# Performance work log

Hardware: AMD Instinct MI355X
Metric: run time of the kernel (lower is better)

## Reference

```python
import jax, jax.numpy as jnp
import numpy as np

B, S, D, H = 2, 2048, 1024, 16
HD = D // H  # head_dim = 64
ROPE_BASE = 10000.0


def setup_inputs() -> dict:
    key = jax.random.key(0)
    ks = jax.random.split(key, 5)
    scale = 1.0 / np.sqrt(D)
    return {
        "x": jax.random.normal(ks[0], (B, S, D), dtype=jnp.float32),
        "Wq": jax.random.normal(ks[1], (D, D), dtype=jnp.float32) * scale,
        "Wk": jax.random.normal(ks[2], (D, D), dtype=jnp.float32) * scale,
        "Wv": jax.random.normal(ks[3], (D, D), dtype=jnp.float32) * scale,
        "Wo": jax.random.normal(ks[4], (D, D), dtype=jnp.float32) * scale,
    }


def _rotate_half(x):
    x1, x2 = x[..., : HD // 2], x[..., HD // 2:]
    return jnp.concatenate((-x2, x1), axis=-1)


def _rope_cos_sin(seq_len):
    inv_freq = 1.0 / (ROPE_BASE ** (jnp.arange(0, HD, 2, dtype=jnp.float32) / HD))
    t = jnp.arange(seq_len, dtype=jnp.float32)
    freqs = jnp.outer(t, inv_freq)          # [S, HD/2]
    emb = jnp.concatenate((freqs, freqs), -1)  # [S, HD]
    return jnp.cos(emb), jnp.sin(emb)


def reference(x, Wq, Wk, Wv, Wo):
    # projections (torch Linear: y = x @ W.T), split heads -> [B, H, S, HD]
    def proj(W):
        return (x @ W.T).reshape(B, S, H, HD).transpose(0, 2, 1, 3)

    q, k, v = proj(Wq), proj(Wk), proj(Wv)

    cos, sin = _rope_cos_sin(S)  # [S, HD] each, broadcast over B, H
    q = q * cos + _rotate_half(q) * sin
    k = k * cos + _rotate_half(k) * sin

    scale = 1.0 / np.sqrt(HD)
    scores = jnp.einsum("bhsd,bhtd->bhst", q, k) * scale  # [B,H,S,S]
    attn = jax.nn.softmax(scores, axis=-1)
    out = jnp.einsum("bhst,bhtd->bhsd", attn, v)           # [B,H,S,HD]
    out = out.transpose(0, 2, 1, 3).reshape(B, S, D)
    return out @ Wo.T
```

## Files before the change

### kernel.cpp

```cpp
#include <hip/hip_runtime.h>
#include <hip/hip_bf16.h>
#include <math.h>
#include <stdint.h>

typedef __bf16 bf16;
typedef __bf16 bf16x8 __attribute__((ext_vector_type(8)));
typedef __bf16 bf16x4 __attribute__((ext_vector_type(4)));
typedef float  f32x4  __attribute__((ext_vector_type(4)));
typedef float  f32x16 __attribute__((ext_vector_type(16)));
typedef unsigned int u32x4 __attribute__((ext_vector_type(4)));

#define MFMA16(a,b,c) __builtin_amdgcn_mfma_f32_16x16x32_bf16((a),(b),(c),0,0,0)
#define MFMA32(a,b,c) __builtin_amdgcn_mfma_f32_32x32x16_bf16((a),(b),(c),0,0,0)

static constexpr int kB  = 2;
static constexpr int kS  = 2048;
static constexpr int kD  = 1024;
static constexpr int kH  = 16;
static constexpr int kHD = 64;
static constexpr int kM  = kB * kS;
static constexpr float kExpC = 0.125f * 1.44269504f;

__device__ __forceinline__ void gl_lds16(const bf16* g, bf16* l) {
  __builtin_amdgcn_global_load_lds(
      (const __attribute__((address_space(1))) unsigned int*)g,
      (__attribute__((address_space(3))) unsigned int*)l, 16, 0, 0);
}

__device__ __forceinline__ unsigned cvt_pk_bf16(float lo, float hi) {
  unsigned r;
  asm("v_cvt_pk_bf16_f32 %0, %1, %2" : "=v"(r) : "v"(lo), "v"(hi));
  return r;
}

__global__ void cvt_all(const float* __restrict__ x,
                        const float* __restrict__ wq, const float* __restrict__ wk,
                        const float* __restrict__ wv, const float* __restrict__ wo,
                        bf16* __restrict__ xb,
                        bf16* __restrict__ wqb, bf16* __restrict__ wkb,
                        bf16* __restrict__ wvb, bf16* __restrict__ wob,
                        float2* __restrict__ rtab)
{
  const int i = blockIdx.x * 256 + threadIdx.x;
  const int NX4 = (kM * kD) / 4;
  const int NW4 = (kD * kD) / 4;
  if (i >= NX4 + 4 * NW4) {
    const int idx = i - (NX4 + 4 * NW4);
    const int s = idx >> 5, d = idx & 31;
    const float f = exp2f(-(float)d * 0.4152410118609203f);
    float sn, cs;
    sincosf((float)s * f, &sn, &cs);
    rtab[idx] = make_float2(cs, sn);
    return;
  }
  const float* src; bf16* dst; int off;
  if (i < NX4) { src = x; dst = xb; off = i; }
  else {
    const int j = i - NX4;
    const int seg = j >> 18;
    off = j & (NW4 - 1);
    src = (seg == 0) ? wq : (seg == 1) ? wk : (seg == 2) ? wv : wo;
    dst = (seg == 0) ? wqb : (seg == 1) ? wkb : (seg == 2) ? wvb : wob;
  }
  const float4 v = ((const float4*)src)[off];
  bf16x4 o = { (bf16)v.x, (bf16)v.y, (bf16)v.z, (bf16)v.w };
  ((bf16x4*)dst)[off] = o;
}

__device__ __forceinline__ void gemm_core_128(
    const bf16* __restrict__ A, const bf16* __restrict__ Bw,
    int m0, int n0, int K, bf16* smem, f32x4 acc[4][4])
{
  const int t = threadIdx.x, lane = t & 63, wave = t >> 6;
  const int wm = wave >> 1, wn = wave & 1;
  const int srow = lane >> 2;
  const int scol = (lane & 3) * 8;
  const bf16* ga0 = A  + (size_t)(m0 + wave * 16 + srow) * K + scol;
  const bf16* ga1 = ga0 + (size_t)64 * K;
  const bf16* gb0 = Bw + (size_t)(n0 + wave * 16 + srow) * K + scol;
  const bf16* gb1 = gb0 + (size_t)64 * K;
  const int woff = wave * 512;

  {
    bf16* lb = smem;
    gl_lds16(ga0, lb + woff);
    gl_lds16(ga1, lb + 2048 + woff);
    gl_lds16(gb0, lb + 4096 + woff);
    gl_lds16(gb1, lb + 6144 + woff);
  }
  int cur = 0;
  for (int k0 = 0; k0 < K; k0 += 32) {
    __syncthreads();
    if (k0 + 32 < K) {
      bf16* lb = smem + (cur ^ 1) * 8192;
      gl_lds16(ga0 + k0 + 32, lb + woff);
      gl_lds16(ga1 + k0 + 32, lb + 2048 + woff);
      gl_lds16(gb0 + k0 + 32, lb + 4096 + woff);
      gl_lds16(gb1 + k0 + 32, lb + 6144 + woff);
    }
    const bf16* aT = smem + cur * 8192;
    const bf16* bT = aT + 4096;
    bf16x8 af[4], bfr[4];
#pragma unroll
    for (int i = 0; i < 4; ++i) {
      af[i]  = *(const bf16x8*)(aT + (wm * 64 + i * 16 + (lane & 15)) * 32 + (lane >> 4) * 8);
      bfr[i] = *(const bf16x8*)(bT + (wn * 64 + i * 16 + (lane & 15)) * 32 + (lane >> 4) * 8);
    }
#pragma unroll
    for (int i = 0; i < 4; ++i)
#pragma unroll
      for (int j = 0; j < 4; ++j)
        acc[i][j] = MFMA16(af[i], bfr[j], acc[i][j]);
    cur ^= 1;
  }
}

__global__ __launch_bounds__(256, 4) void proj_qkv(
    const bf16* __restrict__ xb,
    const bf16* __restrict__ wqb, const bf16* __restrict__ wkb, const bf16* __restrict__ wvb,
    bf16* __restrict__ Qb, bf16* __restrict__ Kb, bf16* __restrict__ Vt,
    const float2* __restrict__ rtab)
{
  __shared__ __align__(16) bf16 smem[16384];
  const int z = blockIdx.z;
  const bf16* Ww = (z == 0) ? wqb : (z == 1) ? wkb : wvb;
  const int m0 = blockIdx.x * 128, n0 = blockIdx.y * 128;
  f32x4 acc[4][4] = {};
  gemm_core_128(xb, Ww, m0, n0, kD, smem, acc);

  const int lane = threadIdx.x & 63, wave = threadIdx.x >> 6;
  const int wm = wave >> 1, wn = wave & 1, quad = lane >> 4, lc = lane & 15;
  const int hh = (n0 >> 6) + wn;
  if (z == 2) {
    __syncthreads();
    const int t = threadIdx.x;
    const int row = t >> 1;
    const int coff = (t & 1) * 32;
    const int bidx = m0 >> 11;
    const int hh2 = (n0 >> 6) + (row >> 6);
    const int d = row & 63;
    bf16* vtr = smem;
#pragma unroll
    for (int p = 0; p < 2; ++p) {
      if (p) __syncthreads();
      if (wm == p) {
#pragma unroll
        for (int i = 0; i < 4; ++i)
#pragma unroll
          for (int j = 0; j < 4; ++j) {
            bf16x4 pk;
#pragma unroll
            for (int r = 0; r < 4; ++r) pk[r] = (bf16)acc[i][j][r];
            *(bf16x4*)&vtr[(wn * 64 + j * 16 + lc) * 72 + i * 16 + quad * 4] = pk;
          }
      }
      __syncthreads();
      bf16* dst = Vt + ((size_t)(bidx * kH + hh2) * kHD + d) * kS
                     + (m0 & 2047) + p * 64 + coff;
#pragma unroll
      for (int u = 0; u < 4; ++u)
        *(uint4*)(dst + u * 8) = *(const uint4*)&vtr[row * 72 + coff + u * 8];
    }
  } else {
    bf16* Op = (z == 0) ? Qb : Kb;
    const float f = (z == 0) ? kExpC : 1.0f;
#pragma unroll
    for (int j = 0; j < 2; ++j) {
      const int d = j * 16 + lc;
#pragma unroll
      for (int i = 0; i < 4; ++i)
#pragma unroll
        for (int r = 0; r < 4; ++r) {
          const int m = m0 + wm * 64 + i * 16 + quad * 4 + r;
          const int bidx = m >> 11, s = m & 2047;
          const float2 cs = rtab[s * 32 + d];
          const float v0 = acc[i][j][r], v1 = acc[i][j + 2][r];
          bf16* dst = Op + ((size_t)(bidx * kH + hh) * kS + s) * kHD;
          dst[d]      = (bf16)((v0 * cs.x - v1 * cs.y) * f);
          dst[d + 32] = (bf16)((v1 * cs.x + v0 * cs.y) * f);
        }
    }
  }
}

__global__ __launch_bounds__(256, 2) void attn(
    const bf16* __restrict__ Qb, const bf16* __restrict__ Kb,
    const bf16* __restrict__ Vt, bf16* __restrict__ Ob)
{
  __shared__ __align__(16) bf16 kT2[2][128 * 64];
  __shared__ __align__(16) bf16 vT2[2][64 * 128];
  const int t = threadIdx.x, lane = t & 63, wave = t >> 6;
  const int l31 = lane & 31, hi = lane >> 5;
  const int bid = blockIdx.x;
  const int qt = (bid >> 3) & 15;
  const int bh = (bid & 7) * 4 + (bid >> 7);
  const size_t base = (size_t)bh * kS * kHD;
  const bf16* Qp = Qb + base + (size_t)qt * 128 * kHD;
  const bf16* Kp = Kb + base;
  const bf16* Vp = Vt + base;

  bf16x8 qf[4];
#pragma unroll
  for (int ks = 0; ks < 4; ++ks)
    qf[ks] = *(const bf16x8*)(Qp + (size_t)(wave * 32 + l31) * kHD + ks * 16 + hi * 8);

  f32x16 oacc[2] = {};
  float lsum = 0.f;

  const bf16* kst  = Kp + (size_t)(wave * 32 + (lane >> 3)) * kHD
                        + 8 * ((lane & 7) ^ (lane >> 3));
  const bf16* vst0 = Vp + (size_t)(wave * 16 + (lane >> 4)) * kS
                        + 8 * ((lane & 15) ^ (lane >> 4));
  const bf16* vst1 = Vp + (size_t)(wave * 16 + (lane >> 4)) * kS
                        + 8 * (((lane & 15) ^ (lane >> 4)) ^ 4);
  const int ldsb = wave * 2048;

#pragma unroll
  for (int i = 0; i < 4; ++i) {
    gl_lds16(kst + (size_t)i * 8 * kHD, &kT2[0][ldsb + i * 512]);
    gl_lds16(((i & 1) ? vst1 : vst0) + (size_t)i * 4 * kS, &vT2[0][ldsb + i * 512]);
  }

  int cur = 0;
  const int NT = kS / 128;
  for (int kt = 0; kt < NT; ++kt) {
    __syncthreads();
    if (kt + 1 < NT) {
      const bf16* kn = kst + (size_t)(kt + 1) * 128 * kHD;
      const int vo = (kt + 1) * 128;
#pragma unroll
      for (int i = 0; i < 4; ++i) {
        gl_lds16(kn + (size_t)i * 8 * kHD, &kT2[cur ^ 1][ldsb + i * 512]);
        gl_lds16(((i & 1) ? vst1 : vst0) + (size_t)i * 4 * kS + vo,
                 &vT2[cur ^ 1][ldsb + i * 512]);
      }
    }
    const bf16* kbuf = kT2[cur];
    const bf16* vbuf = vT2[cur];

    f32x16 sacc[4] = {};
#pragma unroll
    for (int knb = 0; knb < 4; ++knb)
#pragma unroll
      for (int ks = 0; ks < 4; ++ks) {
        const bf16x8 kf = *(const bf16x8*)&kbuf[(knb * 32 + l31) * 64
                                               + 8 * ((ks * 2 + hi) ^ (lane & 7))];
        sacc[knb] = MFMA32(kf, qf[ks], sacc[knb]);
      }

    bf16x8 pfrag[8];
#pragma unroll
    for (int knb = 0; knb < 4; ++knb) {
      float pe[16];
#pragma unroll
      for (int r = 0; r < 16; ++r) pe[r] = __builtin_amdgcn_exp2f(sacc[knb][r]);
      lsum += (((pe[0] + pe[1]) + (pe[2] + pe[3])) + ((pe[4] + pe[5]) + (pe[6] + pe[7])))
            + (((pe[8] + pe[9]) + (pe[10] + pe[11])) + ((pe[12] + pe[13]) + (pe[14] + pe[15])));
#pragma unroll
      for (int h2 = 0; h2 < 2; ++h2) {
        unsigned a0 = cvt_pk_bf16(pe[8 * h2 + 0], pe[8 * h2 + 1]);
        unsigned a1 = cvt_pk_bf16(pe[8 * h2 + 2], pe[8 * h2 + 3]);
        unsigned b0 = cvt_pk_bf16(pe[8 * h2 + 4], pe[8 * h2 + 5]);
        unsigned b1 = cvt_pk_bf16(pe[8 * h2 + 6], pe[8 * h2 + 7]);
        asm("v_permlane32_swap_b32 %0, %1" : "+v"(a0), "+v"(b0));
        asm("v_permlane32_swap_b32 %0, %1" : "+v"(a1), "+v"(b1));
        u32x4 w; w.x = a0; w.y = a1; w.z = b0; w.w = b1;
        pfrag[knb * 2 + h2] = __builtin_bit_cast(bf16x8, w);
      }
    }

#pragma unroll
    for (int nb = 0; nb < 2; ++nb)
#pragma unroll
      for (int tt = 0; tt < 8; ++tt) {
        const bf16x8 vf = *(const bf16x8*)&vbuf[(nb * 32 + l31) * 128
                                               + 8 * ((tt * 2 + hi) ^ (lane & 7))];
        oacc[nb] = MFMA32(vf, pfrag[tt], oacc[nb]);
      }
    cur ^= 1;
  }

  __syncthreads();
  const float total = lsum + __shfl_xor(lsum, 32);
  const float inv = 1.0f / total;
  bf16* tb = &kT2[0][0] + wave * 2304;
#pragma unroll
  for (int nb = 0; nb < 2; ++nb)
#pragma unroll
    for (int rq = 0; rq < 4; ++rq) {
      bf16x4 p4;
#pragma unroll
      for (int e = 0; e < 4; ++e) p4[e] = (bf16)(oacc[nb][rq * 4 + e] * inv);
      *(bf16x4*)&tb[l31 * 72 + nb * 32 + rq * 8 + hi * 4] = p4;
    }
  asm volatile("s_waitcnt lgkmcnt(0)" ::: "memory");
  const int b = bh >> 4, h = bh & 15;
  const int q = lane >> 1, hf = lane & 1;
  const bf16* srcl = &tb[q * 72 + hf * 32];
  bf16* dst = Ob + ((size_t)(b * kS + qt * 128 + wave * 32 + q)) * kD + h * kHD + hf * 32;
#pragma unroll
  for (int u = 0; u < 4; ++u)
    *(uint4*)(dst + u * 8) = *(const uint4*)(srcl + u * 8);
}

__global__ __launch_bounds__(256, 4) void out_proj(
    const bf16* __restrict__ Ab, const bf16* __restrict__ wob, float* __restrict__ Cout)
{
  __shared__ __align__(16) bf16 smem[16384];
  const int m0 = blockIdx.x * 128, n0 = blockIdx.y * 128;
  f32x4 acc[4][4] = {};
  gemm_core_128(Ab, wob, m0, n0, kD, smem, acc);
  const int lane = threadIdx.x & 63, wave = threadIdx.x >> 6;
  const int wm = wave >> 1, wn = wave & 1, quad = lane >> 4, lc = lane & 15;
#pragma unroll
  for (int i = 0; i < 4; ++i)
#pragma unroll
    for (int r = 0; r < 4; ++r) {
      const int m = m0 + wm * 64 + i * 16 + quad * 4 + r;
#pragma unroll
      for (int j = 0; j < 4; ++j)
        Cout[(size_t)m * kD + n0 + wn * 64 + j * 16 + lc] = acc[i][j][r];
    }
}

extern "C" void kernel_launch(void* const* d_in, const int* in_sizes, int n_in,
                              void* d_out, int out_size, void* d_ws, size_t ws_size,
                              hipStream_t stream)
{
  const float* x  = (const float*)d_in[0];
  const float* wq = (const float*)d_in[1];
  const float* wk = (const float*)d_in[2];
  const float* wv = (const float*)d_in[3];
  const float* wo = (const float*)d_in[4];
  float* out = (float*)d_out;

  char* ws = (char*)d_ws;
  const size_t MB = 1024 * 1024;
  if (ws_size < 57 * MB) return;
  bf16* xb  = (bf16*)(ws + 0 * MB);
  bf16* wqb = (bf16*)(ws + 8 * MB);
  bf16* wkb = (bf16*)(ws + 10 * MB);
  bf16* wvb = (bf16*)(ws + 12 * MB);
  bf16* wob = (bf16*)(ws + 14 * MB);
  bf16* Qb  = (bf16*)(ws + 16 * MB);
  bf16* Kb  = (bf16*)(ws + 24 * MB);
  bf16* Ob  = (bf16*)(ws + 40 * MB);
  float2* rtab = (float2*)(ws + 48 * MB);
  bf16* Vtp = (bf16*)(ws + 49 * MB);

  cvt_all<<<8448, 256, 0, stream>>>(x, wq, wk, wv, wo, xb, wqb, wkb, wvb, wob, rtab);
  proj_qkv<<<dim3(32, 8, 3), 256, 0, stream>>>(xb, wqb, wkb, wvb, Qb, Kb, Vtp, rtab);
  attn<<<dim3(512), 256, 0, stream>>>(Qb, Kb, Vtp, Ob);
  out_proj<<<dim3(32, 8), 256, 0, stream>>>(Ob, wob, out);
}
```

Measured before the change: 178.1 us.

## Split attention key tiles across two wave groups with LDS reduction

Each attention block now runs 512 threads. Waves are split into two halves that each process half of every 128-key tile against the same 32 query rows, and each wave loads half as much K/V per stage. At the end, the second half writes its partial output accumulators and row sums into LDS, and the first half adds them before normalizing and storing. The aim is more waves in flight per CU and shorter per-wave dependency chains, at the cost of an extra reduction pass, another barrier, and heavier register and LDS pressure.

```diff
diff --git a/kernel.cpp b/kernel.cpp
--- a/kernel.cpp
+++ b/kernel.cpp
@@ -183,14 +183,14 @@
   }
 }
 
-__global__ __launch_bounds__(256, 2) void attn(
+__global__ __launch_bounds__(512, 4) void attn(
     const bf16* __restrict__ Qb, const bf16* __restrict__ Kb,
     const bf16* __restrict__ Vt, bf16* __restrict__ Ob)
 {
-  __shared__ __align__(16) bf16 kT2[2][128 * 64];
-  __shared__ __align__(16) bf16 vT2[2][64 * 128];
+  __shared__ __align__(16) bf16 lds[32768];
   const int t = threadIdx.x, lane = t & 63, wave = t >> 6;
   const int l31 = lane & 31, hi = lane >> 5;
+  const int qg = wave & 3, kh = wave >> 2;
   const int bid = blockIdx.x;
   const int qt = (bid >> 3) & 15;
   const int bh = (bid & 7) * 4 + (bid >> 7);
@@ -202,24 +202,25 @@
   bf16x8 qf[4];
 #pragma unroll
   for (int ks = 0; ks < 4; ++ks)
-    qf[ks] = *(const bf16x8*)(Qp + (size_t)(wave * 32 + l31) * kHD + ks * 16 + hi * 8);
+    qf[ks] = *(const bf16x8*)(Qp + (size_t)(qg * 32 + l31) * kHD + ks * 16 + hi * 8);
 
   f32x16 oacc[2] = {};
   float lsum = 0.f;
 
-  const bf16* kst  = Kp + (size_t)(wave * 32 + (lane >> 3)) * kHD
+  const bf16* kst  = Kp + (size_t)(wave * 16 + (lane >> 3)) * kHD
                         + 8 * ((lane & 7) ^ (lane >> 3));
-  const bf16* vst0 = Vp + (size_t)(wave * 16 + (lane >> 4)) * kS
+  const bf16* vst0 = Vp + (size_t)(wave * 8 + (lane >> 4)) * kS
                         + 8 * ((lane & 15) ^ (lane >> 4));
-  const bf16* vst1 = Vp + (size_t)(wave * 16 + (lane >> 4)) * kS
-                        + 8 * (((lane & 15) ^ (lane >> 4)) ^ 4);
-  const int ldsb = wave * 2048;
-
-#pragma unroll
-  for (int i = 0; i < 4; ++i) {
-    gl_lds16(kst + (size_t)i * 8 * kHD, &kT2[0][ldsb + i * 512]);
-    gl_lds16(((i & 1) ? vst1 : vst0) + (size_t)i * 4 * kS, &vT2[0][ldsb + i * 512]);
-  }
+  const bf16* vst1 = Vp + (size_t)(wave * 8 + 4 + (lane >> 4)) * kS
+                        + 8 * ((lane & 15) ^ (4 + (lane >> 4)));
+  const int ldsb = wave * 1024;
+  bf16* const kbase = lds;
+  bf16* const vbase = lds + 16384;
+
+  gl_lds16(kst,           kbase + ldsb);
+  gl_lds16(kst + 8 * kHD, kbase + ldsb + 512);
+  gl_lds16(vst0,          vbase + ldsb);
+  gl_lds16(vst1,          vbase + ldsb + 512);
 
   int cur = 0;
   const int NT = kS / 128;
@@ -228,29 +229,27 @@
     if (kt + 1 < NT) {
       const bf16* kn = kst + (size_t)(kt + 1) * 128 * kHD;
       const int vo = (kt + 1) * 128;
-#pragma unroll
-      for (int i = 0; i < 4; ++i) {
-        gl_lds16(kn + (size_t)i * 8 * kHD, &kT2[cur ^ 1][ldsb + i * 512]);
-        gl_lds16(((i & 1) ? vst1 : vst0) + (size_t)i * 4 * kS + vo,
-                 &vT2[cur ^ 1][ldsb + i * 512]);
-      }
-    }
-    const bf16* kbuf = kT2[cur];
-    const bf16* vbuf = vT2[cur];
-
-    f32x16 sacc[4] = {};
-#pragma unroll
-    for (int knb = 0; knb < 4; ++knb)
+      gl_lds16(kn,           kbase + (cur ^ 1) * 8192 + ldsb);
+      gl_lds16(kn + 8 * kHD, kbase + (cur ^ 1) * 8192 + ldsb + 512);
+      gl_lds16(vst0 + vo,    vbase + (cur ^ 1) * 8192 + ldsb);
+      gl_lds16(vst1 + vo,    vbase + (cur ^ 1) * 8192 + ldsb + 512);
+    }
+    const bf16* kbuf = kbase + cur * 8192;
+    const bf16* vbuf = vbase + cur * 8192;
+
+    f32x16 sacc[2] = {};
+#pragma unroll
+    for (int knb = 0; knb < 2; ++knb)
 #pragma unroll
       for (int ks = 0; ks < 4; ++ks) {
-        const bf16x8 kf = *(const bf16x8*)&kbuf[(knb * 32 + l31) * 64
+        const bf16x8 kf = *(const bf16x8*)&kbuf[(kh * 64 + knb * 32 + l31) * 64
                                                + 8 * ((ks * 2 + hi) ^ (lane & 7))];
         sacc[knb] = MFMA32(kf, qf[ks], sacc[knb]);
       }
 
-    bf16x8 pfrag[8];
-#pragma unroll
-    for (int knb = 0; knb < 4; ++knb) {
+    bf16x8 pfrag[4];
+#pragma unroll
+    for (int knb = 0; knb < 2; ++knb) {
       float pe[16];
 #pragma unroll
       for (int r = 0; r < 16; ++r) pe[r] = __builtin_amdgcn_exp2f(sacc[knb][r]);
@@ -272,35 +271,61 @@
 #pragma unroll
     for (int nb = 0; nb < 2; ++nb)
 #pragma unroll
-      for (int tt = 0; tt < 8; ++tt) {
+      for (int tt = 0; tt < 4; ++tt) {
         const bf16x8 vf = *(const bf16x8*)&vbuf[(nb * 32 + l31) * 128
-                                               + 8 * ((tt * 2 + hi) ^ (lane & 7))];
+                                               + 8 * (((kh * 4 + tt) * 2 + hi) ^ (lane & 7))];
         oacc[nb] = MFMA32(vf, pfrag[tt], oacc[nb]);
       }
     cur ^= 1;
   }
 
   __syncthreads();
-  const float total = lsum + __shfl_xor(lsum, 32);
-  const float inv = 1.0f / total;
-  bf16* tb = &kT2[0][0] + wave * 2304;
-#pragma unroll
-  for (int nb = 0; nb < 2; ++nb)
-#pragma unroll
-    for (int rq = 0; rq < 4; ++rq) {
-      bf16x4 p4;
-#pragma unroll
-      for (int e = 0; e < 4; ++e) p4[e] = (bf16)(oacc[nb][rq * 4 + e] * inv);
-      *(bf16x4*)&tb[l31 * 72 + nb * 32 + rq * 8 + hi * 4] = p4;
-    }
-  asm volatile("s_waitcnt lgkmcnt(0)" ::: "memory");
-  const int b = bh >> 4, h = bh & 15;
-  const int q = lane >> 1, hf = lane & 1;
-  const bf16* srcl = &tb[q * 72 + hf * 32];
-  bf16* dst = Ob + ((size_t)(b * kS + qt * 128 + wave * 32 + q)) * kD + h * kHD + hf * 32;
-#pragma unroll
-  for (int u = 0; u < 4; ++u)
-    *(uint4*)(dst + u * 8) = *(const uint4*)(srcl + u * 8);
+  float* red = (float*)lds;
+  const int ridx = (qg * 64 + lane) * 36;
+  if (kh) {
+#pragma unroll
+    for (int nb = 0; nb < 2; ++nb)
+#pragma unroll
+      for (int c = 0; c < 4; ++c) {
+        f32x4 v4;
+#pragma unroll
+        for (int e = 0; e < 4; ++e) v4[e] = oacc[nb][c * 4 + e];
+        *(f32x4*)&red[ridx + nb * 16 + c * 4] = v4;
+      }
+    red[ridx + 32] = lsum;
+  }
+  __syncthreads();
+  if (kh == 0) {
+#pragma unroll
+    for (int nb = 0; nb < 2; ++nb)
+#pragma unroll
+      for (int c = 0; c < 4; ++c) {
+        const f32x4 v4 = *(const f32x4*)&red[ridx + nb * 16 + c * 4];
+#pragma unroll
+        for (int e = 0; e < 4; ++e) oacc[nb][c * 4 + e] += v4[e];
+      }
+    lsum += red[ridx + 32];
+    const float total = lsum + __shfl_xor(lsum, 32);
+    const float inv = 1.0f / total;
+    bf16* tb = lds + 20480 + qg * 2304;
+#pragma unroll
+    for (int nb = 0; nb < 2; ++nb)
+#pragma unroll
+      for (int rq = 0; rq < 4; ++rq) {
+        bf16x4 p4;
+#pragma unroll
+        for (int e = 0; e < 4; ++e) p4[e] = (bf16)(oacc[nb][rq * 4 + e] * inv);
+        *(bf16x4*)&tb[l31 * 72 + nb * 32 + rq * 8 + hi * 4] = p4;
+      }
+    asm volatile("s_waitcnt lgkmcnt(0)" ::: "memory");
+    const int b = bh >> 4, h = bh & 15;
+    const int q = lane >> 1, hf = lane & 1;
+    const bf16* srcl = &tb[q * 72 + hf * 32];
+    bf16* dst = Ob + ((size_t)(b * kS + qt * 128 + qg * 32 + q)) * kD + h * kHD + hf * 32;
+#pragma unroll
+    for (int u = 0; u < 4; ++u)
+      *(uint4*)(dst + u * 8) = *(const uint4*)(srcl + u * 8);
+  }
 }
 
 __global__ __launch_bounds__(256, 4) void out_proj(
@@ -350,6 +375,6 @@
 
   cvt_all<<<8448, 256, 0, stream>>>(x, wq, wk, wv, wo, xb, wqb, wkb, wvb, wob, rtab);
   proj_qkv<<<dim3(32, 8, 3), 256, 0, stream>>>(xb, wqb, wkb, wvb, Qb, Kb, Vtp, rtab);
-  attn<<<dim3(512), 256, 0, stream>>>(Qb, Kb, Vtp, Ob);
+  attn<<<dim3(512), 512, 0, stream>>>(Qb, Kb, Vtp, Ob);
   out_proj<<<dim3(32, 8), 256, 0, stream>>>(Ob, wob, out);
 }
```

New measurement: 175.7 us, median of 2. Within noise of the previous version (-1.4%).
